# Kernel tuning notes

Hardware: AMD Instinct MI355X
Metric: run time of the kernel (lower is better)

## Reference

```python
import jax, jax.numpy as jnp
import numpy as np

B, N, DE, DH, L, DC = 8, 256, 768, 192, 2, 192
NEG = 1e30  # mask_logic constant from the repo


def setup_inputs() -> dict:
    ks = iter(jax.random.split(jax.random.key(0), 32))

    def nrm(shape, s=0.02):
        return jax.random.normal(next(ks), shape, dtype=jnp.float32) * s

    features = jax.random.normal(next(ks), (B, N, DE), dtype=jnp.float32)
    # DAG adjacency: node i attends to a subset of j < i; guarantee edge (i, i-1)
    rnd = jax.random.bernoulli(next(ks), 0.3, (B, N, N))
    tril = jnp.tril(jnp.ones((N, N), jnp.bool_), -1)
    adj = ((rnd & tril[None]) | jnp.eye(N, k=-1, dtype=jnp.bool_)[None]).astype(jnp.float32)
    s_mask = jax.random.bernoulli(next(ks), 0.5, (B, N, N)).astype(jnp.float32)
    s_mask_onehot = jnp.stack([1.0 - s_mask, s_mask], axis=-1)  # unused in forward
    lengths = jnp.full((B,), N, dtype=jnp.int32)  # unused (nodal_att_type=None)
    return dict(
        features=features, adj=adj, s_mask=s_mask,
        s_mask_onehot=s_mask_onehot, lengths=lengths,
        fc1_w=nrm((DE, DH)), fc1_b=jnp.zeros((DH,), jnp.float32),
        gat_w=nrm((L, 2 * DH)), gat_b=jnp.zeros((L,), jnp.float32),
        wr0=nrm((L, DH, DH)), wr1=nrm((L, DH, DH)),
        gruc_wih=nrm((L, 3 * DH, DH)), gruc_whh=nrm((L, 3 * DH, DH)),
        gruc_bih=jnp.zeros((L, 3 * DH), jnp.float32),
        gruc_bhh=jnp.zeros((L, 3 * DH), jnp.float32),
        grup_wih=nrm((L, 3 * DH, DH)), grup_whh=nrm((L, 3 * DH, DH)),
        grup_bih=jnp.zeros((L, 3 * DH), jnp.float32),
        grup_bhh=jnp.zeros((L, 3 * DH), jnp.float32),
        mlp_w0=nrm((DH * (L + 1), DH)), mlp_b0=jnp.zeros((DH,), jnp.float32),
        mlp_w1=nrm((DH, DH)), mlp_b1=jnp.zeros((DH,), jnp.float32),
        mlp_w2=nrm((DH, DC)), mlp_b2=jnp.zeros((DC,), jnp.float32),
    )


def _gru(x, h, wih, whh, bih, bhh):
    # torch.nn.GRUCell math
    gi = x @ wih.T + bih
    gh = h @ whh.T + bhh
    ir, iz, inn = jnp.split(gi, 3, axis=-1)
    hr, hz, hn = jnp.split(gh, 3, axis=-1)
    r = jax.nn.sigmoid(ir + hr)
    z = jax.nn.sigmoid(iz + hz)
    n = jnp.tanh(inn + r * hn)
    return (1.0 - z) * n + z * h


def _layer(Hl, adj, s_mask, gat_w, gat_b, wr0, wr1, cw, cp):
    # One DAG layer: sequential scan over nodes. Carry holds the relation-
    # projected value buffers V0=H1@Wr0^T, V1=H1@Wr1^T and per-node key
    # scores Ksc=H1@wk (rows >= i are zero and masked out), which is
    # mathematically identical to the torch code that re-projects the
    # growing H1 every step.
    wq, wk = gat_w[:DH], gat_w[DH:]
    pos = jnp.arange(N)

    def step(carry, xs):
        V0, V1, Ksc = carry
        i, x_i, adj_i, sm_i = xs  # x_i:(B,DH) adj_i,sm_i:(B,N)
        score = (x_i @ wq)[:, None] + Ksc + gat_b          # (B,N)
        mask = (pos < i)[None, :] & (adj_i > 0.5)          # ragged :i slice
        alpha = jnp.where(mask, score, score - NEG)        # mask_logic
        attn = jax.nn.softmax(alpha, axis=-1)              # masked -> exactly 0
        Vrel = V0 * sm_i[..., None] + V1 * (1.0 - sm_i[..., None])
        M = jnp.einsum('bn,bnd->bd', attn, Vrel)
        M = jnp.where(i > 0, M, 0.0)                       # node 0: no context
        C = _gru(x_i, M, *cw)
        P = _gru(M, x_i, *cp)
        Hnew = C + P
        V0 = V0.at[:, i, :].set(Hnew @ wr0.T)
        V1 = V1.at[:, i, :].set(Hnew @ wr1.T)
        Ksc = Ksc.at[:, i].set(Hnew @ wk)
        attn_out = jnp.where(i > 0, attn, 0.0)             # adjB row 0 is zeros
        return (V0, V1, Ksc), (Hnew, attn_out)

    z3 = jnp.zeros((B, N, DH), jnp.float32)
    carry0 = (z3, z3, jnp.zeros((B, N), jnp.float32))
    xs = (pos, Hl.transpose(1, 0, 2), adj.transpose(1, 0, 2), s_mask.transpose(1, 0, 2))
    _, (Hseq, Aseq) = jax.lax.scan(step, carry0, xs)
    return Hseq.transpose(1, 0, 2), Aseq.transpose(1, 0, 2)  # (B,N,DH),(B,N,N)


def reference(features, adj, s_mask, s_mask_onehot, lengths,
              fc1_w, fc1_b, gat_w, gat_b, wr0, wr1,
              gruc_wih, gruc_whh, gruc_bih, gruc_bhh,
              grup_wih, grup_whh, grup_bih, grup_bhh,
              mlp_w0, mlp_b0, mlp_w1, mlp_b1, mlp_w2, mlp_b2):
    Hl = jax.nn.relu(features @ fc1_w + fc1_b)  # H0
    Hs, As = [Hl], []
    for l in range(L):
        cw = (gruc_wih[l], gruc_whh[l], gruc_bih[l], gruc_bhh[l])
        cp = (grup_wih[l], grup_whh[l], grup_bih[l], grup_bhh[l])
        Hl, Al = _layer(Hl, adj, s_mask, gat_w[l], gat_b[l], wr0[l], wr1[l], cw, cp)
        Hs.append(Hl)
        As.append(Al)
    H = jnp.concatenate(Hs, axis=2)  # (B,N,DH*(L+1))
    # nodal_att_type=None => attentive_node_features is identity
    h = jax.nn.relu(H @ mlp_w0 + mlp_b0)
    h = jax.nn.relu(h @ mlp_w1 + mlp_b1)  # mlp_layers-1 = 1 extra block
    logits = h @ mlp_w2 + mlp_b2          # dropout: eval-mode identity
    return logits, jnp.stack(As, axis=1)  # (B,N,DC), (B,L,N,N)
```

## Files before the change

kernel.cpp:

```cpp
#include <hip/hip_runtime.h>
#include <stdint.h>

#define B_  8
#define N_  256
#define DH_ 192
#define L_  2
#define G3  576
#define G6  1152
#define NW  4
#define DS  48
#define KD  24
#define GC  288
#define STH 10001
#define STP 20001
#define STQ 25001
#define SPK 50000
#define SF1 50001
#define SF2 50002
#define SDN 60001

typedef unsigned long long u64;

__device__ __forceinline__ float bflo(uint32_t u) { return __uint_as_float(u << 16); }
__device__ __forceinline__ float bfhi(uint32_t u) { return __uint_as_float(u & 0xffff0000u); }
__device__ __forceinline__ uint32_t f2bf(float f) {
    uint32_t x = __float_as_uint(f);
    x += 0x7fffu + ((x >> 16) & 1u);
    return x >> 16;
}
__device__ __forceinline__ float sigm(float x)  { return 1.f / (1.f + __expf(-x)); }
__device__ __forceinline__ float tanhf_(float x){ return 1.f - 2.f / (1.f + __expf(2.f * x)); }
__device__ __forceinline__ u64 packvs(float v, int st) {
    return ((u64)(uint32_t)st << 32) | __float_as_uint(v);
}
__device__ __forceinline__ u64 agload(const u64* p) {
    return __hip_atomic_load(p, __ATOMIC_RELAXED, __HIP_MEMORY_SCOPE_AGENT);
}
__device__ __forceinline__ void agstore(u64* p, u64 v) {
    __hip_atomic_store(p, v, __ATOMIC_RELAXED, __HIP_MEMORY_SCOPE_AGENT);
}

struct ScanSm {
    uint4 Wr4s[12 * DH_];
    float sA0[2][N_], sA1[2][N_], sKsc[N_];
    float sAdjN[N_], sSmN[N_];
    float sXq[DH_], sPre[6 * DS], sXv[DS];
    float sM[DH_], su0[DS], su1[DS], sGc[GC], sHn[DS];
    float sRedS[2][4], sRedX[3], sSaved[4];
};
struct WorkSm {
    float sX[DH_];
    float sPv[GC];
    float sRed[3];
};
struct PrologSm {
    float sA[8][768];
    float sRed[3][8][192];
};
struct MlpSm {
    float sH[8][576];
    float sRed[3][8][192];
    float sT[8][192];
};
union SmemAll { ScanSm s; WorkSm w; PrologSm p; MlpSm m; };

__device__ void prepack_slice(int idx,
    const float* __restrict__ wr0, const float* __restrict__ wr1,
    const float* __restrict__ c_wih, const float* __restrict__ c_whh,
    const float* __restrict__ c_bih, const float* __restrict__ c_bhh,
    const float* __restrict__ p_wih, const float* __restrict__ p_whh,
    const float* __restrict__ p_bih, const float* __restrict__ p_bhh,
    float* __restrict__ WpreT, uint32_t* __restrict__ W4,
    uint32_t* __restrict__ Wr4, uint32_t* __restrict__ Wp4w,
    float* __restrict__ biasPre, float* __restrict__ gbx)
{
    for (int l = 0; l < L_; ++l) {
        const float* cwih = c_wih + l * G3 * DH_;
        const float* cwhh = c_whh + l * G3 * DH_;
        const float* pwih = p_wih + l * G3 * DH_;
        const float* pwhh = p_whh + l * G3 * DH_;
        if (l == 0) {
            int k = idx / G6, r = idx - k * G6;
            float w = (r < G3) ? cwih[r * DH_ + k] : pwhh[(r - G3) * DH_ + k];
            WpreT[k * G6 + r] = w;
        }
        if (idx < NW * 27648) {
            int w = idx / 27648, pos = idx % 27648;
            int p4 = pos / 1152, rem = pos % 1152;
            int c2 = rem >> 2, s = rem & 3;
            int p = 4 * p4 + s;
            int j = c2 / DS, dd = c2 % DS;
            int c = 192 * j + DS * w + dd;
            float w0 = (c < G3) ? cwhh[c * DH_ + 2 * p]     : pwih[(c - G3) * DH_ + 2 * p];
            float w1 = (c < G3) ? cwhh[c * DH_ + 2 * p + 1] : pwih[(c - G3) * DH_ + 2 * p + 1];
            W4[l * NW * 27648 + idx] = f2bf(w0) | (f2bf(w1) << 16);
            if (l == 1) {
                int r = c;
                float v0 = (r < G3) ? cwih[r * DH_ + 2 * p]     : pwhh[(r - G3) * DH_ + 2 * p];
                float v1 = (r < G3) ? cwih[r * DH_ + 2 * p + 1] : pwhh[(r - G3) * DH_ + 2 * p + 1];
                Wp4w[idx] = f2bf(v0) | (f2bf(v1) << 16);
            }
        }
        if (idx < NW * 9216) {
            int w = idx / 9216, pos = idx % 9216;
            int kq = pos / 768, rem = pos % 768;
            int d = rem >> 2, s = rem & 3;
            int k = DS * w + 4 * kq + s;
            Wr4[l * NW * 9216 + idx] =
                f2bf(wr0[l * DH_ * DH_ + d * DH_ + k]) |
                (f2bf(wr1[l * DH_ * DH_ + d * DH_ + k]) << 16);
        }
        if (idx < G6) {
            float base = (idx < G3) ? c_bih[l * G3 + idx] : p_bhh[l * G3 + idx - G3];
            float fold = 0.f;
            if (idx < 384)                    fold = c_bhh[l * G3 + idx];
            else if (idx >= G3 && idx < 960)  fold = p_bih[l * G3 + idx - G3];
            biasPre[l * G6 + idx] = base + fold;
        }
        if (idx < 384) {
            gbx[l * 384 + idx] = (idx < DH_) ? c_bhh[l * G3 + 384 + idx]
                                             : p_bih[l * G3 + 384 + (idx - DH_)];
        }
    }
}

__device__ void flag_sync(u64* flags, int wgid, int t, int stamp)
{
    __threadfence();
    __syncthreads();
    if (t == 0) agstore(&flags[wgid], packvs(0.f, stamp));
    if (t < 96) {
        while ((uint32_t)(agload(&flags[t]) >> 32) != (uint32_t)stamp) {}
    }
    __syncthreads();
    __threadfence();
    __syncthreads();
}

__device__ void prologue(char* smem, int wgid, int t,
    const float* __restrict__ features, const float* __restrict__ fc1_w,
    const float* __restrict__ fc1_b, const float* __restrict__ WpreT,
    const float* __restrict__ biasPre,
    float* __restrict__ Hcat, float* __restrict__ PREg, u64* __restrict__ Fp)
{
    PrologSm* P = (PrologSm*)smem;
    const int c = t % 192, kg = t / 192;
    for (int tt = wgid; tt < 256; tt += 96) {
        const int r0 = tt * 8;
        for (int q = t; q < 1536; q += 576) {
            int r = q / 192, c4 = q % 192;
            *(float4*)&P->sA[r][4 * c4] = *(const float4*)(features + (size_t)(r0 + r) * 768 + 4 * c4);
        }
        __syncthreads();
        {
            const float* bp = fc1_w + (size_t)(kg * 256) * 192 + c;
            float acc[8] = {0.f, 0.f, 0.f, 0.f, 0.f, 0.f, 0.f, 0.f};
            #pragma unroll 8
            for (int kk = 0; kk < 256; ++kk) {
                float bv = bp[(size_t)kk * 192];
                #pragma unroll
                for (int rr = 0; rr < 8; ++rr) acc[rr] += P->sA[rr][kg * 256 + kk] * bv;
            }
            #pragma unroll
            for (int rr = 0; rr < 8; ++rr) P->sRed[kg][rr][c] = acc[rr];
        }
        __syncthreads();
        if (t < 192) {
            float bv = fc1_b[t];
            #pragma unroll
            for (int rr = 0; rr < 8; ++rr) {
                float v = P->sRed[0][rr][t] + P->sRed[1][rr][t] + P->sRed[2][rr][t] + bv;
                Hcat[(size_t)(r0 + rr) * G3 + t] = fmaxf(v, 0.f);
            }
        }
        __syncthreads();
    }
    flag_sync(Fp + 96, wgid, t, SF1);
    {
        const float bpa = biasPre[t], bpb = biasPre[576 + t];
        for (int tt = wgid; tt < 256; tt += 96) {
            const int r0 = tt * 8;
            for (int q = t; q < 384; q += 576) {
                int r = q / 48, c4 = q % 48;
                *(float4*)&P->sA[r][4 * c4] = *(const float4*)(Hcat + (size_t)(r0 + r) * G3 + 4 * c4);
            }
            __syncthreads();
            {
                const float* b0 = WpreT + t;
                float a0[8] = {0.f,0.f,0.f,0.f,0.f,0.f,0.f,0.f};
                float a1[8] = {0.f,0.f,0.f,0.f,0.f,0.f,0.f,0.f};
                #pragma unroll 4
                for (int k = 0; k < 192; ++k) {
                    float bva = b0[(size_t)k * G6];
                    float bvb = b0[(size_t)k * G6 + 576];
                    #pragma unroll
                    for (int rr = 0; rr < 8; ++rr) {
                        float av = P->sA[rr][k];
                        a0[rr] += av * bva; a1[rr] += av * bvb;
                    }
                }
                #pragma unroll
                for (int rr = 0; rr < 8; ++rr) {
                    PREg[(size_t)(r0 + rr) * G6 + t]       = a0[rr] + bpa;
                    PREg[(size_t)(r0 + rr) * G6 + 576 + t] = a1[rr] + bpb;
                }
            }
            __syncthreads();
        }
    }
    flag_sync(Fp + 192, wgid, t, SF2);
}

__device__ void mlp_tail(char* smem, int wgid, int t,
    const float* __restrict__ Hcat,
    const float* __restrict__ mw0, const float* __restrict__ mb0,
    const float* __restrict__ mw1, const float* __restrict__ mb1,
    const float* __restrict__ mw2, const float* __restrict__ mb2,
    float* __restrict__ out, u64* __restrict__ Fd)
{
    if (t < 64) {
        while ((uint32_t)(agload(&Fd[t]) >> 32) != (uint32_t)SDN) {}
    }
    __syncthreads();
    __threadfence();
    __syncthreads();
    MlpSm* M = (MlpSm*)smem;
    const int c = t % 192, kg = t / 192;
    for (int tt = wgid; tt < 256; tt += 96) {
        const int r0 = tt * 8;
        for (int q = t; q < 1152; q += 576) {
            int r = q / 144, c4 = q % 144;
            *(float4*)&M->sH[r][4 * c4] = *(const float4*)(Hcat + (size_t)(r0 + r) * G3 + 4 * c4);
        }
        __syncthreads();
        {
            const float* bp = mw0 + (size_t)(kg * 192) * 192 + c;
            float acc[8] = {0.f,0.f,0.f,0.f,0.f,0.f,0.f,0.f};
            #pragma unroll 8
            for (int kk = 0; kk < 192; ++kk) {
                float bv = bp[(size_t)kk * 192];
                #pragma unroll
                for (int rr = 0; rr < 8; ++rr) acc[rr] += M->sH[rr][kg * 192 + kk] * bv;
            }
            #pragma unroll
            for (int rr = 0; rr < 8; ++rr) M->sRed[kg][rr][c] = acc[rr];
        }
        __syncthreads();
        if (t < 192) {
            float bv = mb0[t];
            #pragma unroll
            for (int rr = 0; rr < 8; ++rr)
                M->sT[rr][t] = fmaxf(M->sRed[0][rr][t] + M->sRed[1][rr][t] + M->sRed[2][rr][t] + bv, 0.f);
        }
        __syncthreads();
        {
            const float* bp = mw1 + (size_t)(kg * 64) * 192 + c;
            float acc[8] = {0.f,0.f,0.f,0.f,0.f,0.f,0.f,0.f};
            #pragma unroll 8
            for (int kk = 0; kk < 64; ++kk) {
                float bv = bp[(size_t)kk * 192];
                #pragma unroll
                for (int rr = 0; rr < 8; ++rr) acc[rr] += M->sT[rr][kg * 64 + kk] * bv;
            }
            #pragma unroll
            for (int rr = 0; rr < 8; ++rr) M->sRed[kg][rr][c] = acc[rr];
        }
        __syncthreads();
        if (t < 192) {
            float bv = mb1[t];
            #pragma unroll
            for (int rr = 0; rr < 8; ++rr)
                M->sH[rr][t] = fmaxf(M->sRed[0][rr][t] + M->sRed[1][rr][t] + M->sRed[2][rr][t] + bv, 0.f);
        }
        __syncthreads();
        {
            const float* bp = mw2 + (size_t)(kg * 64) * 192 + c;
            float acc[8] = {0.f,0.f,0.f,0.f,0.f,0.f,0.f,0.f};
            #pragma unroll 8
            for (int kk = 0; kk < 64; ++kk) {
                float bv = bp[(size_t)kk * 192];
                #pragma unroll
                for (int rr = 0; rr < 8; ++rr) acc[rr] += M->sH[rr][kg * 64 + kk] * bv;
            }
            #pragma unroll
            for (int rr = 0; rr < 8; ++rr) M->sRed[kg][rr][c] = acc[rr];
        }
        __syncthreads();
        if (t < 192) {
            float bv = mb2[t];
            #pragma unroll
            for (int rr = 0; rr < 8; ++rr)
                out[(size_t)(r0 + rr) * 192 + t] =
                    M->sRed[0][rr][t] + M->sRed[1][rr][t] + M->sRed[2][rr][t] + bv;
        }
        __syncthreads();
    }
}

template<int ISL2>
__device__ void scan_body(
    ScanSm* S, int b, int w, int t,
    const float* __restrict__ xin, float* __restrict__ hout,
    const float* __restrict__ PREg, const float* __restrict__ adj,
    const float* __restrict__ smask,
    const uint32_t* __restrict__ W4l, const uint32_t* __restrict__ Wr4l,
    const float* __restrict__ gbxl, const float* __restrict__ gatwl,
    uint32_t* __restrict__ Hw, u64* __restrict__ MPsl, u64* __restrict__ Kdl,
    u64* __restrict__ HcW, const u64* __restrict__ HcR,
    const u64* __restrict__ PREcR, const u64* __restrict__ XQcR,
    float* __restrict__ AsB, int sbase)
{
    const int lane = t & 63, wave = t >> 6;
    const int dg0 = w * DS;
    const float* adjB = adj   + (size_t)b * N_ * N_;
    const float* smB  = smask + (size_t)b * N_ * N_;
    const int fi = b * NW;
    const int cB4 = t >> 1, khB4 = t & 1;

    {
        uint32_t* wr = (uint32_t*)S->Wr4s;
        for (int q = t; q < 9216; q += 576) wr[q] = Wr4l[q];
    }
    uint4 wreg[12];
    {
        const uint4* W4v = (const uint4*)W4l;
        #pragma unroll
        for (int p4 = 0; p4 < 12; ++p4) wreg[p4] = W4v[(12 * khB4 + p4) * GC + cB4];
    }
    float wqv = (!ISL2 && t < DH_) ? gatwl[t] : 0.f;
    float wkv = 0.f, g2b = 0.f, g5b = 0.f;
    if (t < DS) { wkv = gatwl[DH_ + dg0 + t]; g2b = gbxl[dg0 + t]; g5b = gbxl[DH_ + dg0 + t]; }
    if (t < N_) { S->sKsc[t] = 0.f; S->sA0[1][t] = 0.f; S->sA1[1][t] = 0.f; }
    if (t < DS) { S->su0[t] = 0.f; S->su1[t] = 0.f; }
    if (t < 4)  S->sRedS[1][t] = 0.f;
    if (w == 0 && t < N_) AsB[t] = 0.f;

    if (!ISL2) {
        if (t < DS) {
            const float* pre = PREg + (size_t)(b * N_) * G6 + dg0 + t;
            S->sPre[t] = pre[0]; S->sPre[DS + t] = pre[192]; S->sPre[2 * DS + t] = pre[384];
            S->sPre[3 * DS + t] = pre[576]; S->sPre[4 * DS + t] = pre[768]; S->sPre[5 * DS + t] = pre[960];
            S->sXv[t] = xin[(size_t)(b * N_) * G3 + dg0 + t];
        }
        for (int q = t; q < 176; q += 576) {
            if (q < 64)       *(float4*)&S->sAdjN[4 * q] = *(const float4*)(adjB + N_ + 4 * q);
            else if (q < 128) { int q2 = q - 64;  *(float4*)&S->sSmN[4 * q2] = *(const float4*)(smB + N_ + 4 * q2); }
            else              { int q2 = q - 128; *(float4*)&S->sXq[4 * q2] = *(const float4*)(xin + (size_t)(b * N_ + 1) * G3 + 4 * q2); }
        }
    } else {
        for (int q = t; q < 321; q += 576) {
            if (q < 64)       *(float4*)&S->sAdjN[4 * q] = *(const float4*)(adjB + N_ + 4 * q);
            else if (q < 128) { int q2 = q - 64;  *(float4*)&S->sSmN[4 * q2] = *(const float4*)(smB + N_ + 4 * q2); }
            else if (q < 176) {
                int d = q - 128;
                const u64* p = HcR + ((size_t)(b * N_) * NW + w) * DS + d;
                u64 v; do { v = agload(p); } while ((uint32_t)(v >> 32) != (uint32_t)STH);
                S->sXv[d] = __uint_as_float((uint32_t)v);
            } else if (q < 320) {
                int qq = q - 176;
                const u64* p = PREcR + ((size_t)(b * N_) * NW + w) * 144 + qq;
                u64 v; do { v = agload(p); } while ((uint32_t)(v >> 32) != (uint32_t)STP);
                uint32_t pl = (uint32_t)v;
                S->sPre[2 * qq] = bflo(pl); S->sPre[2 * qq + 1] = bfhi(pl);
            } else {
                const u64* p = XQcR + b * N_ + 1;
                u64 v; do { v = agload(p); } while ((uint32_t)(v >> 32) != (uint32_t)(STQ + 1));
                S->sSaved[3] = __uint_as_float((uint32_t)v);
            }
        }
    }
    __syncthreads();
    {
        float hn = 0.f;
        if (t < DS) {
            float xv = S->sXv[t];
            float r1 = sigm(S->sPre[t]), z1 = sigm(S->sPre[DS + t]);
            float n1 = tanhf_(S->sPre[2 * DS + t] + r1 * g2b);
            float Cv = (1.f - z1) * n1;
            float r2 = sigm(S->sPre[3 * DS + t]), z2 = sigm(S->sPre[4 * DS + t]);
            float n2 = tanhf_(g5b + r2 * S->sPre[5 * DS + t]);
            hn = Cv + (1.f - z2) * n2 + z2 * xv;
            S->sHn[t] = hn;
            hout[(size_t)(b * N_) * G3 + dg0 + t] = hn;
            if (!ISL2) HcW[((size_t)(b * N_) * NW + w) * DS + t] = packvs(hn, STH);
        }
        if (t == 0) { S->sSaved[0] = S->sAdjN[0]; S->sSaved[1] = S->sSmN[0]; }
        if (wave == 0) {
            float v = hn * wkv;
            #pragma unroll
            for (int o = 32; o; o >>= 1) v += __shfl_xor(v, o);
            if (lane == 0) agstore(&Kdl[fi + w], packvs(v, sbase));
        }
    }
    __syncthreads();
    if (t < KD) Hw[(size_t)t * N_] = f2bf(S->sHn[2 * t]) | (f2bf(S->sHn[2 * t + 1]) << 16);
    if (!ISL2) {
        float px = (t < DH_) ? S->sXq[t] * wqv : 0.f;
        #pragma unroll
        for (int o = 32; o; o >>= 1) px += __shfl_xor(px, o);
        if (t < DH_ && lane == 0) S->sRedX[wave] = px;
    }
    __syncthreads();
    float xqc = ISL2 ? S->sSaved[3] : (S->sRedX[0] + S->sRedX[1] + S->sRedX[2]);

    for (int i = 1; i < N_; ++i) {
        const int row = b * N_ + i;
        const int stamp = sbase + i;
        const int pp = i & 1, pn = pp ^ 1;

        if (t >= 384) {
            const int u = t - 384;
            const int inx = (i + 1 < N_) ? i + 1 : N_ - 1;
            if (!ISL2) {
                for (int qq = u; qq < 260; qq += 192) {
                    if (qq < 64)
                        *(float4*)&S->sAdjN[4 * qq] = *(const float4*)(adjB + (size_t)inx * N_ + 4 * qq);
                    else if (qq < 128) { int q2 = qq - 64;
                        *(float4*)&S->sSmN[4 * q2] = *(const float4*)(smB + (size_t)inx * N_ + 4 * q2); }
                    else if (qq < 140) { int q2 = qq - 128;
                        *(float4*)&S->sXv[4 * q2] = *(const float4*)(xin + (size_t)row * G3 + dg0 + 4 * q2); }
                    else if (qq < 212) { int q2 = qq - 140; int g = q2 / 12, o = q2 - 12 * g;
                        *(float4*)&S->sPre[g * DS + 4 * o] =
                            *(const float4*)(PREg + (size_t)row * G6 + g * DH_ + dg0 + 4 * o); }
                    else { int q2 = qq - 212;
                        *(float4*)&S->sXq[4 * q2] = *(const float4*)(xin + (size_t)(b * N_ + inx) * G3 + 4 * q2); }
                }
            } else {
                for (int qq = u; qq < 321; qq += 192) {
                    if (qq < 64)
                        *(float4*)&S->sAdjN[4 * qq] = *(const float4*)(adjB + (size_t)inx * N_ + 4 * qq);
                    else if (qq < 128) { int q2 = qq - 64;
                        *(float4*)&S->sSmN[4 * q2] = *(const float4*)(smB + (size_t)inx * N_ + 4 * q2); }
                    else if (qq < 176) {
                        int d = qq - 128;
                        const u64* p = HcR + ((size_t)row * NW + w) * DS + d;
                        u64 v; do { v = agload(p); } while ((uint32_t)(v >> 32) != (uint32_t)(STH + i));
                        S->sXv[d] = __uint_as_float((uint32_t)v);
                    } else if (qq < 320) {
                        int q2 = qq - 176;
                        const u64* p = PREcR + ((size_t)row * NW + w) * 144 + q2;
                        u64 v; do { v = agload(p); } while ((uint32_t)(v >> 32) != (uint32_t)(STP + i));
                        uint32_t pl = (uint32_t)v;
                        S->sPre[2 * q2] = bflo(pl); S->sPre[2 * q2 + 1] = bfhi(pl);
                    } else {
                        const u64* p = XQcR + b * N_ + inx;
                        u64 v; do { v = agload(p); } while ((uint32_t)(v >> 32) != (uint32_t)(STQ + inx));
                        S->sSaved[3] = __uint_as_float((uint32_t)v);
                    }
                }
            }
            if (t == 575) {
                const uint32_t ex = (uint32_t)(stamp - 1);
                u64 k0, k1, k2, k3;
                do {
                    k0 = agload(&Kdl[fi + 0]); k1 = agload(&Kdl[fi + 1]);
                    k2 = agload(&Kdl[fi + 2]); k3 = agload(&Kdl[fi + 3]);
                } while ((uint32_t)(k0 >> 32) != ex || (uint32_t)(k1 >> 32) != ex ||
                         (uint32_t)(k2 >> 32) != ex || (uint32_t)(k3 >> 32) != ex);
                float kdot = __uint_as_float((uint32_t)k0) + __uint_as_float((uint32_t)k1)
                           + __uint_as_float((uint32_t)k2) + __uint_as_float((uint32_t)k3);
                float adjI1 = S->sSaved[0], smI1 = S->sSaved[1];
                float e1 = (adjI1 > 0.5f) ? __expf(xqc + kdot) : 0.f;
                float Ssum = S->sRedS[pp][0] + S->sRedS[pp][1] + S->sRedS[pp][2] + S->sRedS[pp][3] + e1;
                S->sKsc[i - 1] = kdot;
                float c0 = e1 * smI1;
                S->sA0[pp][i - 1] = c0; S->sA1[pp][i - 1] = e1 - c0;
                S->sSaved[2] = 1.f / Ssum;
            }
        }
        __syncthreads();

        if (t < DH_) {
            float mp = 0.f, h0a = 0.f, h1a = 0.f;
            #pragma unroll 4
            for (int kq = 0; kq < 12; ++kq) {
                uint4 wv = S->Wr4s[kq * DH_ + t];
                const int k0 = 4 * kq;
                float lo, hi;
                lo = bflo(wv.x); hi = bfhi(wv.x);
                mp = fmaf(S->su0[k0 + 0], lo, mp); mp = fmaf(S->su1[k0 + 0], hi, mp);
                h0a = fmaf(S->sHn[k0 + 0], lo, h0a); h1a = fmaf(S->sHn[k0 + 0], hi, h1a);
                lo = bflo(wv.y); hi = bfhi(wv.y);
                mp = fmaf(S->su0[k0 + 1], lo, mp); mp = fmaf(S->su1[k0 + 1], hi, mp);
                h0a = fmaf(S->sHn[k0 + 1], lo, h0a); h1a = fmaf(S->sHn[k0 + 1], hi, h1a);
                lo = bflo(wv.z); hi = bfhi(wv.z);
                mp = fmaf(S->su0[k0 + 2], lo, mp); mp = fmaf(S->su1[k0 + 2], hi, mp);
                h0a = fmaf(S->sHn[k0 + 2], lo, h0a); h1a = fmaf(S->sHn[k0 + 2], hi, h1a);
                lo = bflo(wv.w); hi = bfhi(wv.w);
                mp = fmaf(S->su0[k0 + 3], lo, mp); mp = fmaf(S->su1[k0 + 3], hi, mp);
                h0a = fmaf(S->sHn[k0 + 3], lo, h0a); h1a = fmaf(S->sHn[k0 + 3], hi, h1a);
            }
            float invS = S->sSaved[2];
            mp = (mp + S->sA0[pp][i - 1] * h0a + S->sA1[pp][i - 1] * h1a) * invS;
            S->sM[t] = mp;
            agstore(&MPsl[(size_t)(fi + w) * DH_ + t], packvs(mp, stamp));
            if (!ISL2) {
                float px = S->sXq[t] * wqv;
                #pragma unroll
                for (int o = 32; o; o >>= 1) px += __shfl_xor(px, o);
                if (lane == 0) S->sRedX[wave] = px;
            }
        } else if (w == 0 && t < 448) {
            int j = t - 192;
            AsB[(size_t)i * N_ + j] = (S->sA0[pp][j] + S->sA1[pp][j]) * S->sSaved[2];
        }
        __syncthreads();

        const float xqn = ISL2 ? S->sSaved[3] : (S->sRedX[0] + S->sRedX[1] + S->sRedX[2]);
        if (t < N_) {
            float e = 0.f;
            if (t == i) { S->sSaved[0] = S->sAdjN[t]; S->sSaved[1] = S->sSmN[t]; }
            if (t < i && S->sAdjN[t] > 0.5f) e = __expf(xqn + S->sKsc[t]);
            float b0 = e * S->sSmN[t];
            S->sA0[pn][t] = b0; S->sA1[pn][t] = e - b0;
            float ps = e;
            #pragma unroll
            for (int o = 32; o; o >>= 1) ps += __shfl_xor(ps, o);
            if (lane == 0) S->sRedS[pn][wave] = ps;
        }
        __syncthreads();

        if (t < 384) {
            const int ilim = i;
            const int kd = t >> 4, jp = t & 15;
            const uint32_t* hp = Hw + (size_t)kd * N_;
            float u0l = 0.f, u0h = 0.f, u1l = 0.f, u1h = 0.f;
            int j = jp;
            while (j + 48 < ilim) {
                uint32_t h0 = hp[j], h1 = hp[j + 16], h2 = hp[j + 32], h3 = hp[j + 48];
                float b0, b1;
                b0 = S->sA0[pn][j];      b1 = S->sA1[pn][j];
                u0l = fmaf(b0, bflo(h0), u0l); u0h = fmaf(b0, bfhi(h0), u0h);
                u1l = fmaf(b1, bflo(h0), u1l); u1h = fmaf(b1, bfhi(h0), u1h);
                b0 = S->sA0[pn][j + 16]; b1 = S->sA1[pn][j + 16];
                u0l = fmaf(b0, bflo(h1), u0l); u0h = fmaf(b0, bfhi(h1), u0h);
                u1l = fmaf(b1, bflo(h1), u1l); u1h = fmaf(b1, bfhi(h1), u1h);
                b0 = S->sA0[pn][j + 32]; b1 = S->sA1[pn][j + 32];
                u0l = fmaf(b0, bflo(h2), u0l); u0h = fmaf(b0, bfhi(h2), u0h);
                u1l = fmaf(b1, bflo(h2), u1l); u1h = fmaf(b1, bfhi(h2), u1h);
                b0 = S->sA0[pn][j + 48]; b1 = S->sA1[pn][j + 48];
                u0l = fmaf(b0, bflo(h3), u0l); u0h = fmaf(b0, bfhi(h3), u0h);
                u1l = fmaf(b1, bflo(h3), u1l); u1h = fmaf(b1, bfhi(h3), u1h);
                j += 64;
            }
            for (; j < ilim; j += 16) {
                uint32_t hv = hp[j];
                float b0 = S->sA0[pn][j], b1 = S->sA1[pn][j];
                u0l = fmaf(b0, bflo(hv), u0l); u0h = fmaf(b0, bfhi(hv), u0h);
                u1l = fmaf(b1, bflo(hv), u1l); u1h = fmaf(b1, bfhi(hv), u1h);
            }
            #pragma unroll
            for (int o = 1; o <= 8; o <<= 1) {
                u0l += __shfl_xor(u0l, o); u0h += __shfl_xor(u0h, o);
                u1l += __shfl_xor(u1l, o); u1h += __shfl_xor(u1h, o);
            }
            if (jp == 0) {
                S->su0[2 * kd] = u0l; S->su0[2 * kd + 1] = u0h;
                S->su1[2 * kd] = u1l; S->su1[2 * kd + 1] = u1h;
            }
        } else {
            const int d = t - 384;
            const int w1 = (w + 1) & 3, w2 = (w + 2) & 3, w3 = (w + 3) & 3;
            u64* pA = &MPsl[(size_t)(fi + w1) * DH_ + d];
            u64* pB = &MPsl[(size_t)(fi + w2) * DH_ + d];
            u64* pC = &MPsl[(size_t)(fi + w3) * DH_ + d];
            const uint32_t ex = (uint32_t)stamp;
            u64 vA, vB, vC;
            do {
                vA = agload(pA); vB = agload(pB); vC = agload(pC);
            } while ((uint32_t)(vA >> 32) != ex || (uint32_t)(vB >> 32) != ex ||
                     (uint32_t)(vC >> 32) != ex);
            S->sM[d] += __uint_as_float((uint32_t)vA)
                      + __uint_as_float((uint32_t)vB)
                      + __uint_as_float((uint32_t)vC);
        }
        __syncthreads();

        {
            float g = 0.f;
            #pragma unroll
            for (int p4 = 0; p4 < 12; ++p4) {
                const uint4 wv = wreg[p4];
                const int m0 = 8 * (12 * khB4 + p4);
                g = fmaf(S->sM[m0 + 0], bflo(wv.x), g); g = fmaf(S->sM[m0 + 1], bfhi(wv.x), g);
                g = fmaf(S->sM[m0 + 2], bflo(wv.y), g); g = fmaf(S->sM[m0 + 3], bfhi(wv.y), g);
                g = fmaf(S->sM[m0 + 4], bflo(wv.z), g); g = fmaf(S->sM[m0 + 5], bfhi(wv.z), g);
                g = fmaf(S->sM[m0 + 6], bflo(wv.w), g); g = fmaf(S->sM[m0 + 7], bfhi(wv.w), g);
            }
            g += __shfl_xor(g, 1);
            if (khB4 == 0) S->sGc[cB4] = g;
        }
        __syncthreads();

        {
            float hn = 0.f;
            if (t < DS) {
                float Mv = S->sM[dg0 + t];
                float r1 = sigm(S->sPre[t] + S->sGc[t]);
                float z1 = sigm(S->sPre[DS + t] + S->sGc[DS + t]);
                float n1 = tanhf_(S->sPre[2 * DS + t] + r1 * (S->sGc[2 * DS + t] + g2b));
                float Cv = (1.f - z1) * n1 + z1 * Mv;
                float r2 = sigm(S->sGc[3 * DS + t] + S->sPre[3 * DS + t]);
                float z2 = sigm(S->sGc[4 * DS + t] + S->sPre[4 * DS + t]);
                float n2 = tanhf_(S->sGc[5 * DS + t] + g5b + r2 * S->sPre[5 * DS + t]);
                hn = Cv + (1.f - z2) * n2 + z2 * S->sXv[t];
                S->sHn[t] = hn;
                hout[(size_t)row * G3 + dg0 + t] = hn;
                if (!ISL2) HcW[((size_t)row * NW + w) * DS + t] = packvs(hn, STH + i);
            }
            if (wave == 0) {
                float v = hn * wkv;
                #pragma unroll
                for (int o = 32; o; o >>= 1) v += __shfl_xor(v, o);
                if (lane == 0) agstore(&Kdl[fi + w], packvs(v, stamp));
            }
            if (t < KD) Hw[(size_t)t * N_ + i] = f2bf(S->sHn[2 * t]) | (f2bf(S->sHn[2 * t + 1]) << 16);
        }
        __syncthreads();
        xqc = xqn;
    }
}

__device__ void worker_body(WorkSm* Wm, int b, int w, int t,
    const uint32_t* __restrict__ Wp4g, const float* __restrict__ bias2,
    const float* __restrict__ wq2,
    const u64* __restrict__ HcR, u64* __restrict__ PREcW, u64* __restrict__ XQcW)
{
    const int lane = t & 63, wave = t >> 6;
    const int c = t >> 1, kh = t & 1;
    uint4 wpreg[12];
    {
        const uint4* v4 = (const uint4*)Wp4g;
        #pragma unroll
        for (int p4 = 0; p4 < 12; ++p4) wpreg[p4] = v4[(12 * kh + p4) * GC + c];
    }
    float bv = 0.f;
    if (kh == 0) bv = bias2[192 * (c / DS) + w * DS + (c % DS)];
    float wqt = (t < DH_) ? wq2[t] : 0.f;
    for (int i = 0; i < N_; ++i) {
        if (t < DH_) {
            const u64* p = HcR + ((size_t)(b * N_ + i) * NW + (t / DS)) * DS + (t % DS);
            u64 v; do { v = agload(p); } while ((uint32_t)(v >> 32) != (uint32_t)(STH + i));
            Wm->sX[t] = __uint_as_float((uint32_t)v);
        }
        __syncthreads();
        {
            float g = 0.f;
            #pragma unroll
            for (int p4 = 0; p4 < 12; ++p4) {
                const uint4 wv = wpreg[p4];
                const int m0 = 8 * (12 * kh + p4);
                g = fmaf(Wm->sX[m0 + 0], bflo(wv.x), g); g = fmaf(Wm->sX[m0 + 1], bfhi(wv.x), g);
                g = fmaf(Wm->sX[m0 + 2], bflo(wv.y), g); g = fmaf(Wm->sX[m0 + 3], bfhi(wv.y), g);
                g = fmaf(Wm->sX[m0 + 4], bflo(wv.z), g); g = fmaf(Wm->sX[m0 + 5], bfhi(wv.z), g);
                g = fmaf(Wm->sX[m0 + 6], bflo(wv.w), g); g = fmaf(Wm->sX[m0 + 7], bfhi(wv.w), g);
            }
            g += __shfl_xor(g, 1);
            if (kh == 0) Wm->sPv[c] = g + bv;
        }
        if (w == 0) {
            float px = (t < DH_) ? Wm->sX[t] * wqt : 0.f;
            #pragma unroll
            for (int o = 32; o; o >>= 1) px += __shfl_xor(px, o);
            if (t < DH_ && lane == 0) Wm->sRed[wave] = px;
        }
        __syncthreads();
        if (t < 144) {
            u64 v = ((u64)(uint32_t)(STP + i) << 32)
                  | f2bf(Wm->sPv[2 * t]) | (f2bf(Wm->sPv[2 * t + 1]) << 16);
            agstore(&PREcW[((size_t)(b * N_ + i) * NW + w) * 144 + t], v);
        }
        if (w == 0 && t == 0)
            agstore(&XQcW[b * N_ + i],
                    packvs(Wm->sRed[0] + Wm->sRed[1] + Wm->sRed[2], STQ + i));
        __syncthreads();
    }
}

__global__ __launch_bounds__(576, 1) void pipeline_kernel(
    const float* __restrict__ features, const float* __restrict__ fc1_w,
    const float* __restrict__ fc1_b,
    const float* __restrict__ adj, const float* __restrict__ smask,
    const float* __restrict__ gatw,
    const float* __restrict__ wr0, const float* __restrict__ wr1,
    const float* __restrict__ c_wih, const float* __restrict__ c_whh,
    const float* __restrict__ c_bih, const float* __restrict__ c_bhh,
    const float* __restrict__ p_wih, const float* __restrict__ p_whh,
    const float* __restrict__ p_bih, const float* __restrict__ p_bhh,
    const float* __restrict__ mw0, const float* __restrict__ mb0,
    const float* __restrict__ mw1, const float* __restrict__ mb1,
    const float* __restrict__ mw2, const float* __restrict__ mb2,
    float* __restrict__ Hcat, float* __restrict__ PREg,
    float* __restrict__ WpreT, uint32_t* __restrict__ W4,
    uint32_t* __restrict__ Wr4, uint32_t* __restrict__ Wp4w,
    float* __restrict__ biasPre, float* __restrict__ gbx,
    uint32_t* __restrict__ Hb, u64* __restrict__ MPs, u64* __restrict__ Kd,
    u64* __restrict__ Hc, u64* __restrict__ PREc, u64* __restrict__ XQc,
    u64* __restrict__ Fp, u64* __restrict__ Fd,
    float* __restrict__ out)
{
    __shared__ __align__(16) char smem[sizeof(SmemAll)];
    const int blk = blockIdx.x, t = threadIdx.x;
    const int wgid = blk;
    const int b = blk & 7, r12 = blk >> 3;
    const int role = r12 >> 2, w = r12 & 3;

    for (int j = 0; j < 4; ++j) {
        int idx = wgid * 576 + t + 55296 * j;
        prepack_slice(idx, wr0, wr1, c_wih, c_whh, c_bih, c_bhh,
                      p_wih, p_whh, p_bih, p_bhh,
                      WpreT, W4, Wr4, Wp4w, biasPre, gbx);
    }
    flag_sync(Fp, wgid, t, SPK);

    prologue(smem, wgid, t, features, fc1_w, fc1_b, WpreT, biasPre,
             Hcat, PREg, Fp);

    float* As = out + 393216;
    if (role == 0) {
        scan_body<0>((ScanSm*)smem, b, w, t,
            Hcat, Hcat + 192, PREg, adj, smask,
            W4, Wr4, gbx, gatw,
            Hb + (size_t)(b * NW + w) * KD * N_, MPs, Kd,
            Hc, nullptr, nullptr, nullptr,
            As + (size_t)b * (L_ * N_ * N_), 1);
        __threadfence();
        __syncthreads();
        if (t == 0) agstore(&Fd[b * 8 + w], packvs(0.f, SDN));
    } else if (role == 2) {
        scan_body<1>((ScanSm*)smem, b, w, t,
            nullptr, Hcat + 384, nullptr, adj, smask,
            W4 + NW * 27648, Wr4 + NW * 9216, gbx + 384, gatw + 384,
            Hb + (size_t)(32 + b * NW + w) * KD * N_,
            MPs + (size_t)8 * NW * DH_, Kd + 8 * NW,
            nullptr, Hc, PREc, XQc,
            As + (size_t)b * (L_ * N_ * N_) + N_ * N_, 30001);
        __threadfence();
        __syncthreads();
        if (t == 0) agstore(&Fd[b * 8 + 4 + w], packvs(0.f, SDN));
    } else {
        worker_body((WorkSm*)smem, b, w, t,
            Wp4w + (size_t)w * 27648, biasPre + G6, gatw + 384,
            Hc, PREc, XQc);
    }

    mlp_tail(smem, wgid, t, Hcat, mw0, mb0, mw1, mb1, mw2, mb2, out, Fd);
}

extern "C" void kernel_launch(void* const* d_in, const int* in_sizes, int n_in,
                              void* d_out, int out_size, void* d_ws, size_t ws_size,
                              hipStream_t stream)
{
    const float* features = (const float*)d_in[0];
    const float* adj      = (const float*)d_in[1];
    const float* smask    = (const float*)d_in[2];
    const float* fc1_w = (const float*)d_in[5];
    const float* fc1_b = (const float*)d_in[6];
    const float* gat_w = (const float*)d_in[7];
    const float* wr0   = (const float*)d_in[9];
    const float* wr1   = (const float*)d_in[10];
    const float* c_wih = (const float*)d_in[11];
    const float* c_whh = (const float*)d_in[12];
    const float* c_bih = (const float*)d_in[13];
    const float* c_bhh = (const float*)d_in[14];
    const float* p_wih = (const float*)d_in[15];
    const float* p_whh = (const float*)d_in[16];
    const float* p_bih = (const float*)d_in[17];
    const float* p_bhh = (const float*)d_in[18];
    const float* mw0 = (const float*)d_in[19];
    const float* mb0 = (const float*)d_in[20];
    const float* mw1 = (const float*)d_in[21];
    const float* mb1 = (const float*)d_in[22];
    const float* mw2 = (const float*)d_in[23];
    const float* mb2 = (const float*)d_in[24];
    float* out = (float*)d_out;

    char* wsb = (char*)d_ws;
    size_t off = 0;
    auto carve = [&](size_t bytes) -> char* {
        char* p = wsb + off;
        off = (off + bytes + 255) & ~(size_t)255;
        return p;
    };
    float* Hcat     = (float*)carve(2048ull * 576 * 4);
    float* PREg     = (float*)carve(2048ull * 1152 * 4);
    float* WpreT    = (float*)carve(192ull * 1152 * 4);
    uint32_t* W4    = (uint32_t*)carve(2ull * NW * 27648 * 4);
    uint32_t* Wr4   = (uint32_t*)carve(2ull * NW * 9216 * 4);
    uint32_t* Wp4w  = (uint32_t*)carve((size_t)NW * 27648 * 4);
    float* biasPre  = (float*)carve(2ull * 1152 * 4);
    float* gbx      = (float*)carve(2ull * 384 * 4);
    uint32_t* Hb    = (uint32_t*)carve(64ull * KD * 256 * 4);
    u64* MPs        = (u64*)carve(2ull * 8 * NW * DH_ * 8);
    u64* Kd         = (u64*)carve(2ull * 8 * NW * 8);
    u64* Hc         = (u64*)carve(8ull * 256 * NW * DS * 8);
    u64* PREc       = (u64*)carve(8ull * 256 * NW * 144 * 8);
    u64* XQc        = (u64*)carve(8ull * 256 * 8);
    u64* Fp         = (u64*)carve(288ull * 8);
    u64* Fd         = (u64*)carve(64ull * 8);

    pipeline_kernel<<<dim3(96), 576, 0, stream>>>(
        features, fc1_w, fc1_b, adj, smask, gat_w,
        wr0, wr1, c_wih, c_whh, c_bih, c_bhh, p_wih, p_whh, p_bih, p_bhh,
        mw0, mb0, mw1, mb1, mw2, mb2,
        Hcat, PREg, WpreT, W4, Wr4, Wp4w, biasPre, gbx,
        Hb, MPs, Kd, Hc, PREc, XQc, Fp, Fd, out);
}
```

Measured before the change: 1.932 ms.

## Restructure DAG scan step to overlap cross-block K exchange with message matmul

Reorders each sequential scan step so the Wr message projection (partial sums rr, p0, p1) is computed and published before waiting on the attention key-dot from the other workgroups. The newest node's attention weight is now folded in afterwards as a rank-one correction. The query prefetch moves two steps ahead with double-buffered sXq, and the Kd and MPs exchange buffers are double-buffered by parity. The goal is to take the cross-workgroup spin-wait and one barrier phase off the critical path of the serial loop. In exchange, each step sends three times as many atomic values between workgroups and adds extra shared-memory state and bookkeeping.

```diff
diff --git a/kernel.cpp b/kernel.cpp
--- a/kernel.cpp
+++ b/kernel.cpp
@@ -11,6 +11,8 @@
 #define DS  48
 #define KD  24
 #define GC  288
+#define MPSZ (8 * NW * DH_ * 3)
+#define KDSZ (8 * NW)
 #define STH 10001
 #define STP 20001
 #define STQ 25001
@@ -39,14 +41,17 @@
 __device__ __forceinline__ void agstore(u64* p, u64 v) {
     __hip_atomic_store(p, v, __ATOMIC_RELAXED, __HIP_MEMORY_SCOPE_AGENT);
 }
+__device__ __forceinline__ float u2f(u64 v) { return __uint_as_float((uint32_t)v); }
 
 struct ScanSm {
     uint4 Wr4s[12 * DH_];
     float sA0[2][N_], sA1[2][N_], sKsc[N_];
     float sAdjN[N_], sSmN[N_];
-    float sXq[DH_], sPre[6 * DS], sXv[DS];
+    float sXq[2][DH_];
+    float sPre[6 * DS], sXv[DS];
     float sM[DH_], su0[DS], su1[DS], sGc[GC], sHn[DS];
-    float sRedS[2][4], sRedX[3], sSaved[4];
+    float sRl[DH_], sP0l[DH_], sP1l[DH_];
+    float sRedS[2][8], sRedX[3], sSaved[8], sSavedA[2], sSavedS[2];
 };
 struct WorkSm {
     float sX[DH_];
@@ -327,12 +332,12 @@
         #pragma unroll
         for (int p4 = 0; p4 < 12; ++p4) wreg[p4] = W4v[(12 * khB4 + p4) * GC + cB4];
     }
-    float wqv = (!ISL2 && t < DH_) ? gatwl[t] : 0.f;
+    float wqx = (!ISL2 && t >= 192 && t < 384) ? gatwl[t - 192] : 0.f;
     float wkv = 0.f, g2b = 0.f, g5b = 0.f;
     if (t < DS) { wkv = gatwl[DH_ + dg0 + t]; g2b = gbxl[dg0 + t]; g5b = gbxl[DH_ + dg0 + t]; }
     if (t < N_) { S->sKsc[t] = 0.f; S->sA0[1][t] = 0.f; S->sA1[1][t] = 0.f; }
     if (t < DS) { S->su0[t] = 0.f; S->su1[t] = 0.f; }
-    if (t < 4)  S->sRedS[1][t] = 0.f;
+    if (t < 5)  S->sRedS[1][t] = 0.f;
     if (w == 0 && t < N_) AsB[t] = 0.f;
 
     if (!ISL2) {
@@ -342,10 +347,11 @@
             S->sPre[3 * DS + t] = pre[576]; S->sPre[4 * DS + t] = pre[768]; S->sPre[5 * DS + t] = pre[960];
             S->sXv[t] = xin[(size_t)(b * N_) * G3 + dg0 + t];
         }
-        for (int q = t; q < 176; q += 576) {
+        for (int q = t; q < 224; q += 576) {
             if (q < 64)       *(float4*)&S->sAdjN[4 * q] = *(const float4*)(adjB + N_ + 4 * q);
             else if (q < 128) { int q2 = q - 64;  *(float4*)&S->sSmN[4 * q2] = *(const float4*)(smB + N_ + 4 * q2); }
-            else              { int q2 = q - 128; *(float4*)&S->sXq[4 * q2] = *(const float4*)(xin + (size_t)(b * N_ + 1) * G3 + 4 * q2); }
+            else if (q < 176) { int q2 = q - 128; *(float4*)&S->sXq[1][4 * q2] = *(const float4*)(xin + (size_t)(b * N_ + 1) * G3 + 4 * q2); }
+            else              { int q2 = q - 176; *(float4*)&S->sXq[0][4 * q2] = *(const float4*)(xin + (size_t)(b * N_ + 2) * G3 + 4 * q2); }
         }
     } else {
         for (int q = t; q < 321; q += 576) {
@@ -384,21 +390,21 @@
             hout[(size_t)(b * N_) * G3 + dg0 + t] = hn;
             if (!ISL2) HcW[((size_t)(b * N_) * NW + w) * DS + t] = packvs(hn, STH);
         }
-        if (t == 0) { S->sSaved[0] = S->sAdjN[0]; S->sSaved[1] = S->sSmN[0]; }
+        if (t == 0) { S->sSavedA[1] = S->sAdjN[0]; S->sSavedS[1] = S->sSmN[0]; }
         if (wave == 0) {
             float v = hn * wkv;
             #pragma unroll
             for (int o = 32; o; o >>= 1) v += __shfl_xor(v, o);
-            if (lane == 0) agstore(&Kdl[fi + w], packvs(v, sbase));
+            if (lane == 0) { S->sSaved[6] = v; agstore(&Kdl[fi + w], packvs(v, sbase)); }
         }
     }
     __syncthreads();
     if (t < KD) Hw[(size_t)t * N_] = f2bf(S->sHn[2 * t]) | (f2bf(S->sHn[2 * t + 1]) << 16);
-    if (!ISL2) {
-        float px = (t < DH_) ? S->sXq[t] * wqv : 0.f;
+    if (!ISL2 && t >= 192 && t < 384) {
+        float px = S->sXq[1][t - 192] * wqx;
         #pragma unroll
         for (int o = 32; o; o >>= 1) px += __shfl_xor(px, o);
-        if (t < DH_ && lane == 0) S->sRedX[wave] = px;
+        if (lane == 0) S->sRedX[wave - 3] = px;
     }
     __syncthreads();
     float xqc = ISL2 ? S->sSaved[3] : (S->sRedX[0] + S->sRedX[1] + S->sRedX[2]);
@@ -408,10 +414,43 @@
         const int stamp = sbase + i;
         const int pp = i & 1, pn = pp ^ 1;
 
-        if (t >= 384) {
+        if (t < DH_) {
+            float rr = 0.f, p0 = 0.f, p1 = 0.f;
+            #pragma unroll 4
+            for (int kq = 0; kq < 12; ++kq) {
+                uint4 wv = S->Wr4s[kq * DH_ + t];
+                const int k0 = 4 * kq;
+                float lo, hi;
+                lo = bflo(wv.x); hi = bfhi(wv.x);
+                rr = fmaf(S->su0[k0 + 0], lo, rr); rr = fmaf(S->su1[k0 + 0], hi, rr);
+                p0 = fmaf(S->sHn[k0 + 0], lo, p0); p1 = fmaf(S->sHn[k0 + 0], hi, p1);
+                lo = bflo(wv.y); hi = bfhi(wv.y);
+                rr = fmaf(S->su0[k0 + 1], lo, rr); rr = fmaf(S->su1[k0 + 1], hi, rr);
+                p0 = fmaf(S->sHn[k0 + 1], lo, p0); p1 = fmaf(S->sHn[k0 + 1], hi, p1);
+                lo = bflo(wv.z); hi = bfhi(wv.z);
+                rr = fmaf(S->su0[k0 + 2], lo, rr); rr = fmaf(S->su1[k0 + 2], hi, rr);
+                p0 = fmaf(S->sHn[k0 + 2], lo, p0); p1 = fmaf(S->sHn[k0 + 2], hi, p1);
+                lo = bflo(wv.w); hi = bfhi(wv.w);
+                rr = fmaf(S->su0[k0 + 3], lo, rr); rr = fmaf(S->su1[k0 + 3], hi, rr);
+                p0 = fmaf(S->sHn[k0 + 3], lo, p0); p1 = fmaf(S->sHn[k0 + 3], hi, p1);
+            }
+            S->sRl[t] = rr; S->sP0l[t] = p0; S->sP1l[t] = p1;
+            u64* base = &MPsl[(size_t)pp * MPSZ + ((size_t)(fi + w) * DH_ + t) * 3];
+            agstore(base + 0, packvs(rr, stamp));
+            agstore(base + 1, packvs(p0, stamp));
+            agstore(base + 2, packvs(p1, stamp));
+        } else if (t < 384) {
+            if (!ISL2) {
+                float px = S->sXq[(i - 1) & 1][t - 192] * wqx;
+                #pragma unroll
+                for (int o = 32; o; o >>= 1) px += __shfl_xor(px, o);
+                if (lane == 0) S->sRedX[wave - 3] = px;
+            }
+        } else {
             const int u = t - 384;
             const int inx = (i + 1 < N_) ? i + 1 : N_ - 1;
             if (!ISL2) {
+                const int ixq = (i + 2 < N_) ? i + 2 : N_ - 1;
                 for (int qq = u; qq < 260; qq += 192) {
                     if (qq < 64)
                         *(float4*)&S->sAdjN[4 * qq] = *(const float4*)(adjB + (size_t)inx * N_ + 4 * qq);
@@ -423,7 +462,7 @@
                         *(float4*)&S->sPre[g * DS + 4 * o] =
                             *(const float4*)(PREg + (size_t)row * G6 + g * DH_ + dg0 + 4 * o); }
                     else { int q2 = qq - 212;
-                        *(float4*)&S->sXq[4 * q2] = *(const float4*)(xin + (size_t)(b * N_ + inx) * G3 + 4 * q2); }
+                        *(float4*)&S->sXq[i & 1][4 * q2] = *(const float4*)(xin + (size_t)(b * N_ + ixq) * G3 + 4 * q2); }
                 }
             } else {
                 for (int qq = u; qq < 321; qq += 192) {
@@ -449,68 +488,14 @@
                     }
                 }
             }
-            if (t == 575) {
-                const uint32_t ex = (uint32_t)(stamp - 1);
-                u64 k0, k1, k2, k3;
-                do {
-                    k0 = agload(&Kdl[fi + 0]); k1 = agload(&Kdl[fi + 1]);
-                    k2 = agload(&Kdl[fi + 2]); k3 = agload(&Kdl[fi + 3]);
-                } while ((uint32_t)(k0 >> 32) != ex || (uint32_t)(k1 >> 32) != ex ||
-                         (uint32_t)(k2 >> 32) != ex || (uint32_t)(k3 >> 32) != ex);
-                float kdot = __uint_as_float((uint32_t)k0) + __uint_as_float((uint32_t)k1)
-                           + __uint_as_float((uint32_t)k2) + __uint_as_float((uint32_t)k3);
-                float adjI1 = S->sSaved[0], smI1 = S->sSaved[1];
-                float e1 = (adjI1 > 0.5f) ? __expf(xqc + kdot) : 0.f;
-                float Ssum = S->sRedS[pp][0] + S->sRedS[pp][1] + S->sRedS[pp][2] + S->sRedS[pp][3] + e1;
-                S->sKsc[i - 1] = kdot;
-                float c0 = e1 * smI1;
-                S->sA0[pp][i - 1] = c0; S->sA1[pp][i - 1] = e1 - c0;
-                S->sSaved[2] = 1.f / Ssum;
-            }
-        }
-        __syncthreads();
-
-        if (t < DH_) {
-            float mp = 0.f, h0a = 0.f, h1a = 0.f;
-            #pragma unroll 4
-            for (int kq = 0; kq < 12; ++kq) {
-                uint4 wv = S->Wr4s[kq * DH_ + t];
-                const int k0 = 4 * kq;
-                float lo, hi;
-                lo = bflo(wv.x); hi = bfhi(wv.x);
-                mp = fmaf(S->su0[k0 + 0], lo, mp); mp = fmaf(S->su1[k0 + 0], hi, mp);
-                h0a = fmaf(S->sHn[k0 + 0], lo, h0a); h1a = fmaf(S->sHn[k0 + 0], hi, h1a);
-                lo = bflo(wv.y); hi = bfhi(wv.y);
-                mp = fmaf(S->su0[k0 + 1], lo, mp); mp = fmaf(S->su1[k0 + 1], hi, mp);
-                h0a = fmaf(S->sHn[k0 + 1], lo, h0a); h1a = fmaf(S->sHn[k0 + 1], hi, h1a);
-                lo = bflo(wv.z); hi = bfhi(wv.z);
-                mp = fmaf(S->su0[k0 + 2], lo, mp); mp = fmaf(S->su1[k0 + 2], hi, mp);
-                h0a = fmaf(S->sHn[k0 + 2], lo, h0a); h1a = fmaf(S->sHn[k0 + 2], hi, h1a);
-                lo = bflo(wv.w); hi = bfhi(wv.w);
-                mp = fmaf(S->su0[k0 + 3], lo, mp); mp = fmaf(S->su1[k0 + 3], hi, mp);
-                h0a = fmaf(S->sHn[k0 + 3], lo, h0a); h1a = fmaf(S->sHn[k0 + 3], hi, h1a);
-            }
-            float invS = S->sSaved[2];
-            mp = (mp + S->sA0[pp][i - 1] * h0a + S->sA1[pp][i - 1] * h1a) * invS;
-            S->sM[t] = mp;
-            agstore(&MPsl[(size_t)(fi + w) * DH_ + t], packvs(mp, stamp));
-            if (!ISL2) {
-                float px = S->sXq[t] * wqv;
-                #pragma unroll
-                for (int o = 32; o; o >>= 1) px += __shfl_xor(px, o);
-                if (lane == 0) S->sRedX[wave] = px;
-            }
-        } else if (w == 0 && t < 448) {
-            int j = t - 192;
-            AsB[(size_t)i * N_ + j] = (S->sA0[pp][j] + S->sA1[pp][j]) * S->sSaved[2];
         }
         __syncthreads();
 
         const float xqn = ISL2 ? S->sSaved[3] : (S->sRedX[0] + S->sRedX[1] + S->sRedX[2]);
         if (t < N_) {
             float e = 0.f;
-            if (t == i) { S->sSaved[0] = S->sAdjN[t]; S->sSaved[1] = S->sSmN[t]; }
-            if (t < i && S->sAdjN[t] > 0.5f) e = __expf(xqn + S->sKsc[t]);
+            if (t == i) { S->sSavedA[pn] = S->sAdjN[t]; S->sSavedS[pn] = S->sSmN[t]; }
+            if (t < i - 1 && S->sAdjN[t] > 0.5f) e = __expf(xqn + S->sKsc[t]);
             float b0 = e * S->sSmN[t];
             S->sA0[pn][t] = b0; S->sA1[pn][t] = e - b0;
             float ps = e;
@@ -521,7 +506,7 @@
         __syncthreads();
 
         if (t < 384) {
-            const int ilim = i;
+            const int ilim = i - 1;
             const int kd = t >> 4, jp = t & 15;
             const uint32_t* hp = Hw + (size_t)kd * N_;
             float u0l = 0.f, u0h = 0.f, u1l = 0.f, u1h = 0.f;
@@ -561,18 +546,65 @@
         } else {
             const int d = t - 384;
             const int w1 = (w + 1) & 3, w2 = (w + 2) & 3, w3 = (w + 3) & 3;
-            u64* pA = &MPsl[(size_t)(fi + w1) * DH_ + d];
-            u64* pB = &MPsl[(size_t)(fi + w2) * DH_ + d];
-            u64* pC = &MPsl[(size_t)(fi + w3) * DH_ + d];
+            const u64* pA = &MPsl[(size_t)pp * MPSZ + ((size_t)(fi + w1) * DH_ + d) * 3];
+            const u64* pB = &MPsl[(size_t)pp * MPSZ + ((size_t)(fi + w2) * DH_ + d) * 3];
+            const u64* pC = &MPsl[(size_t)pp * MPSZ + ((size_t)(fi + w3) * DH_ + d) * 3];
             const uint32_t ex = (uint32_t)stamp;
-            u64 vA, vB, vC;
+            u64 a0, a1, a2, b0, b1, b2, c0, c1, c2;
             do {
-                vA = agload(pA); vB = agload(pB); vC = agload(pC);
-            } while ((uint32_t)(vA >> 32) != ex || (uint32_t)(vB >> 32) != ex ||
-                     (uint32_t)(vC >> 32) != ex);
-            S->sM[d] += __uint_as_float((uint32_t)vA)
-                      + __uint_as_float((uint32_t)vB)
-                      + __uint_as_float((uint32_t)vC);
+                a0 = agload(pA); a1 = agload(pA + 1); a2 = agload(pA + 2);
+                b0 = agload(pB); b1 = agload(pB + 1); b2 = agload(pB + 2);
+                c0 = agload(pC); c1 = agload(pC + 1); c2 = agload(pC + 2);
+            } while ((uint32_t)(a0 >> 32) != ex || (uint32_t)(a1 >> 32) != ex ||
+                     (uint32_t)(a2 >> 32) != ex || (uint32_t)(b0 >> 32) != ex ||
+                     (uint32_t)(b1 >> 32) != ex || (uint32_t)(b2 >> 32) != ex ||
+                     (uint32_t)(c0 >> 32) != ex || (uint32_t)(c1 >> 32) != ex ||
+                     (uint32_t)(c2 >> 32) != ex);
+            S->sRl[d]  += u2f(a0) + u2f(b0) + u2f(c0);
+            S->sP0l[d] += u2f(a1) + u2f(b1) + u2f(c1);
+            S->sP1l[d] += u2f(a2) + u2f(b2) + u2f(c2);
+            if (t == 575) {
+                const uint32_t ex2 = (uint32_t)(stamp - 1);
+                const int kpar = (i - 1) & 1;
+                u64 k0, k1, k2;
+                u64* q1 = &Kdl[kpar * KDSZ + fi + w1];
+                u64* q2 = &Kdl[kpar * KDSZ + fi + w2];
+                u64* q3 = &Kdl[kpar * KDSZ + fi + w3];
+                do {
+                    k0 = agload(q1); k1 = agload(q2); k2 = agload(q3);
+                } while ((uint32_t)(k0 >> 32) != ex2 || (uint32_t)(k1 >> 32) != ex2 ||
+                         (uint32_t)(k2 >> 32) != ex2);
+                float kdot = S->sSaved[6] + u2f(k0) + u2f(k1) + u2f(k2);
+                float adj1 = S->sSavedA[pp], sm1 = S->sSavedS[pp];
+                float e1 = (adj1 > 0.5f) ? __expf(xqc + kdot) : 0.f;
+                float Ssum = S->sRedS[pp][0] + S->sRedS[pp][1] + S->sRedS[pp][2]
+                           + S->sRedS[pp][3] + S->sRedS[pp][4] + e1;
+                S->sKsc[i - 1] = kdot;
+                float invS = 1.f / Ssum;
+                float e1c0 = e1 * sm1, e1c1 = e1 - e1c0;
+                S->sSaved[2] = invS;
+                S->sSaved[4] = e1c0; S->sSaved[5] = e1c1;
+                S->sA0[pp][i - 1] = e1c0; S->sA1[pp][i - 1] = e1c1;
+                float adjn = S->sAdjN[i - 1], smn = S->sSmN[i - 1];
+                float en = (adjn > 0.5f) ? __expf(xqn + kdot) : 0.f;
+                float n0 = en * smn;
+                S->sA0[pn][i - 1] = n0; S->sA1[pn][i - 1] = en - n0;
+                S->sRedS[pn][4] = en;
+            }
+        }
+        __syncthreads();
+
+        if (t < DH_) {
+            S->sM[t] = (S->sRl[t] + S->sSaved[4] * S->sP0l[t]
+                                  + S->sSaved[5] * S->sP1l[t]) * S->sSaved[2];
+        } else if (t < 192 + DS) {
+            const int k = t - 192;
+            float a0 = S->sA0[pn][i - 1], a1 = S->sA1[pn][i - 1];
+            S->su0[k] += a0 * S->sHn[k];
+            S->su1[k] += a1 * S->sHn[k];
+        } else if (w == 0 && t >= 256 && t < 512) {
+            const int j = t - 256;
+            AsB[(size_t)i * N_ + j] = (S->sA0[pp][j] + S->sA1[pp][j]) * S->sSaved[2];
         }
         __syncthreads();
 
@@ -612,7 +644,7 @@
                 float v = hn * wkv;
                 #pragma unroll
                 for (int o = 32; o; o >>= 1) v += __shfl_xor(v, o);
-                if (lane == 0) agstore(&Kdl[fi + w], packvs(v, stamp));
+                if (lane == 0) { S->sSaved[6] = v; agstore(&Kdl[pp * KDSZ + fi + w], packvs(v, stamp)); }
             }
             if (t < KD) Hw[(size_t)t * N_ + i] = f2bf(S->sHn[2 * t]) | (f2bf(S->sHn[2 * t + 1]) << 16);
         }
@@ -732,7 +764,7 @@
             nullptr, Hcat + 384, nullptr, adj, smask,
             W4 + NW * 27648, Wr4 + NW * 9216, gbx + 384, gatw + 384,
             Hb + (size_t)(32 + b * NW + w) * KD * N_,
-            MPs + (size_t)8 * NW * DH_, Kd + 8 * NW,
+            MPs + (size_t)2 * MPSZ, Kd + 2 * KDSZ,
             nullptr, Hc, PREc, XQc,
             As + (size_t)b * (L_ * N_ * N_) + N_ * N_, 30001);
         __threadfence();
@@ -791,8 +823,8 @@
     float* biasPre  = (float*)carve(2ull * 1152 * 4);
     float* gbx      = (float*)carve(2ull * 384 * 4);
     uint32_t* Hb    = (uint32_t*)carve(64ull * KD * 256 * 4);
-    u64* MPs        = (u64*)carve(2ull * 8 * NW * DH_ * 8);
-    u64* Kd         = (u64*)carve(2ull * 8 * NW * 8);
+    u64* MPs        = (u64*)carve(4ull * MPSZ * 8);
+    u64* Kd         = (u64*)carve(4ull * KDSZ * 8);
     u64* Hc         = (u64*)carve(8ull * 256 * NW * DS * 8);
     u64* PREc       = (u64*)carve(8ull * 256 * NW * 144 * 8);
     u64* XQc        = (u64*)carve(8ull * 256 * 8);
```

Measured after the change: 1.737 ms. 1.11x faster.
